# Kernel optimization log

Hardware: AMD Instinct MI355X
Metric: run time of the kernel (lower is better)

## Reference

```python
import jax, jax.numpy as jnp
import numpy as np
from jax import lax

B, CIN, HID, T, H, W = 4, 32, 32, 31, 96, 96


def setup_inputs() -> dict:
    key = jax.random.key(0)
    k1, k2, k3 = jax.random.split(key, 3)
    inputs = jax.random.normal(k1, (B, CIN, T, H, W), dtype=jnp.float32)
    conv_w = jax.random.normal(k2, (2 * HID, CIN, 3, 3, 3), dtype=jnp.float32) * 0.05
    conv_b = jax.random.normal(k3, (2 * HID,), dtype=jnp.float32) * 0.05
    gamma = jnp.ones((1,), dtype=jnp.float32)
    return {"inputs": inputs, "conv_w": conv_w, "conv_b": conv_b, "gamma": gamma}


def reference(inputs, conv_w, conv_b, gamma):
    hid = conv_w.shape[0] // 2
    # Conv3d, 'same' padding, NCDHW layout -> gates [B, 2*hid, T, H, W]
    gates = lax.conv_general_dilated(
        inputs, conv_w, window_strides=(1, 1, 1), padding="SAME",
        dimension_numbers=("NCDHW", "OIDHW", "NCDHW"))
    gates = gates + conv_b[None, :, None, None, None]
    Z = jnp.tanh(gates[:, :hid])          # [B, hid, T, H, W]
    F = jax.nn.sigmoid(gates[:, hid:])    # [B, hid, T, H, W]

    # Gated recurrence over time (dim 2): h_t = f_t * h_{t-1} + (1 - f_t) * z_t
    Zt = jnp.moveaxis(Z, 2, 0)  # [T, B, hid, H, W]
    Ft = jnp.moveaxis(F, 2, 0)

    def step(h, zf):
        z, f = zf
        h = f * h + (1.0 - f) * z
        return h, h

    h0 = jnp.zeros_like(Zt[0])  # h=None <=> h0=0 since f*0+(1-f)*z
    _, hs = lax.scan(step, h0, (Zt, Ft))
    h_time = jnp.moveaxis(hs, 0, 2)  # [B, hid, T, H, W]

    # Per-spatial-location channel attention
    qh = jnp.transpose(h_time, (0, 3, 4, 1, 2))  # [B, H, W, C, T]
    scores = jnp.einsum("bhwct,bhwdt->bhwcd", qh, qh)  # [B, H, W, C, C]
    attn = jax.nn.softmax(scores, axis=3)  # softmax over row axis c (dim=3), as in torch
    attn = attn * (1.0 / np.sqrt(qh.shape[-2]))  # divide AFTER softmax by sqrt(C)
    ah = jnp.einsum("bhwcd,bhwdt->bhwct", attn, qh)  # [B, H, W, C, T]
    ah = jnp.transpose(ah, (0, 3, 4, 1, 2))  # [B, C, T, H, W]

    return gamma * ah + h_time
```

## Files before the change

### kernel.cpp

```cpp
#include <hip/hip_runtime.h>
#include <math.h>

#define B_ 4
#define CIN_ 32
#define HID_ 32
#define T_ 31
#define H_ 96
#define W_ 96
#define SP_ (H_*W_)
#define TSP (T_ * SP_)

typedef _Float16 half8 __attribute__((ext_vector_type(8)));
typedef float f32x4 __attribute__((ext_vector_type(4)));
typedef float f32x16 __attribute__((ext_vector_type(16)));

static __device__ inline unsigned int packhh(float a, float b) {
  unsigned short ua = __builtin_bit_cast(unsigned short, (_Float16)a);
  unsigned short ub = __builtin_bit_cast(unsigned short, (_Float16)b);
  return (unsigned int)ua | ((unsigned int)ub << 16);
}

__global__ __launch_bounds__(256) void prep_w_kernel(
    const float* __restrict__ w, _Float16* __restrict__ wr) {
  int idx = blockIdx.x * 256 + threadIdx.x;
  if (idx >= 55296) return;
  int i = idx & 7;
  int lane = (idx >> 3) & 63;
  int rest = idx >> 9;
  int tap = rest % 27;
  int ocg = rest / 27;
  int m = lane & 15;
  int cin = (lane >> 4) * 8 + i;
  int oc = (m & 1) * 32 + ocg * 8 + (m >> 1);
  wr[idx] = (_Float16)(w[(oc * CIN_ + cin) * 27 + tap]);
}

#define PITCH 40
#define SROWS 8
#define SCOLS 18
#define RST (SCOLS * PITCH)
#define SLICE_HF (SROWS * RST)

__global__ __launch_bounds__(256, 2) void conv_rec_mfma(
    const float* __restrict__ in, const _Float16* __restrict__ wr,
    const float* __restrict__ bias, unsigned int* __restrict__ gout) {
  __shared__ _Float16 in_s[4 * SLICE_HF];

  const int tid = threadIdx.x;
  const int tile = blockIdx.x;
  const int b = blockIdx.y;
  const int x0 = (tile % 6) * 16;
  const int y0 = (tile / 6) * 6;
  const int lane = tid & 63;
  const int ocg = tid >> 6;
  const int px = lane & 15;
  const int kq = lane >> 4;

  half8 wreg[27];
  {
    const _Float16* wp = wr + (size_t)ocg * 27 * 512 + lane * 8;
#pragma unroll
    for (int tap = 0; tap < 27; ++tap)
      wreg[tap] = *(const half8*)(wp + tap * 512);
  }

  const int c0 = ocg * 8 + 2 * kq;
  f32x4 bias4;
  bias4[0] = bias[c0];
  bias4[1] = bias[32 + c0];
  bias4[2] = bias[c0 + 1];
  bias4[3] = bias[32 + c0 + 1];

  const int s_xi = tid & 15;
  const int s_q  = tid >> 4;
  const int ibase = s_q * TSP + (y0 - 1) * W_ + x0 + s_xi;
  const int wbase = (s_xi + 1) * PITCH + s_q;
  const int e_cin = tid & 31;
  const int e_yy  = tid >> 5;
  const int e_gy  = y0 - 1 + e_yy;
  const bool e_ok = ((unsigned)e_gy < (unsigned)H_);
  const int eoff  = e_cin * TSP + e_gy * W_;
  const int ew0   = e_yy * RST + 0 * PITCH + e_cin;
  const int ew1   = e_yy * RST + 17 * PITCH + e_cin;
  const bool has_l = (x0 > 0), has_r = (x0 + 16 < W_);

  int cs[3];
#pragma unroll
  for (int kw = 0; kw < 3; ++kw) cs[kw] = (px + kw) * PITCH + kq * 8;

  const float* inb = in + (size_t)(b * CIN_) * TSP;

  auto stage_full = [&](int ts) {
    _Float16* dst = in_s + (ts & 3) * SLICE_HF;
    const int tso = ts * SP_;
#pragma unroll
    for (int k = 0; k < 16; ++k) {
      const int gy = y0 - 1 + (k >> 1);
      float v = 0.f;
      if ((unsigned)gy < (unsigned)H_)
        v = inb[ibase + (k & 1) * 16 * TSP + (k >> 1) * W_ + tso];
      dst[wbase + (k >> 1) * RST + (k & 1) * 16] = (_Float16)v;
    }
    float v0 = 0.f, v1 = 0.f;
    if (e_ok) {
      if (has_l) v0 = inb[eoff + tso + x0 - 1];
      if (has_r) v1 = inb[eoff + tso + x0 + 16];
    }
    dst[ew0] = (_Float16)v0;
    dst[ew1] = (_Float16)v1;
  };

  {
    uint32_t* dz = (uint32_t*)(in_s + 3 * SLICE_HF);
    for (int e = tid; e < SLICE_HF / 2; e += 256) dz[e] = 0u;
  }
  stage_full(0);
  stage_full(1);
  __syncthreads();

  float h[6][2];
#pragma unroll
  for (int r = 0; r < 6; ++r) { h[r][0] = 0.f; h[r][1] = 0.f; }

  const int pr = ocg * 4 + kq;
  size_t obase = ((size_t)(b * 32 + pr) * T_) * SP_ + y0 * W_ + x0 + px;

  for (int t = 0; t < T_; ++t) {
    const int ts = t + 2;

    float sv[16], ev0 = 0.f, ev1 = 0.f;
    if (ts < T_) {
      const int tso = ts * SP_;
#pragma unroll
      for (int k = 0; k < 16; ++k) {
        const int gy = y0 - 1 + (k >> 1);
        sv[k] = 0.f;
        if ((unsigned)gy < (unsigned)H_)
          sv[k] = inb[ibase + (k & 1) * 16 * TSP + (k >> 1) * W_ + tso];
      }
      if (e_ok) {
        if (has_l) ev0 = inb[eoff + tso + x0 - 1];
        if (has_r) ev1 = inb[eoff + tso + x0 + 16];
      }
    }

    f32x4 acc[6];
#pragma unroll
    for (int r = 0; r < 6; ++r) acc[r] = bias4;

#pragma unroll
    for (int kd = 0; kd < 3; ++kd) {
      const _Float16* sb2 = in_s + ((t + 3 + kd) & 3) * SLICE_HF;
#pragma unroll
      for (int kw = 0; kw < 3; ++kw) {
        half8 brow[8];
#pragma unroll
        for (int rr = 0; rr < 8; ++rr)
          brow[rr] = *(const half8*)(sb2 + rr * RST + cs[kw]);
#pragma unroll
        for (int kh = 0; kh < 3; ++kh) {
          const int tap = kd * 9 + kh * 3 + kw;
#pragma unroll
          for (int r = 0; r < 6; ++r)
            acc[r] = __builtin_amdgcn_mfma_f32_16x16x32_f16(
                wreg[tap], brow[r + kh], acc[r], 0, 0, 0);
        }
      }
    }

    if (ts < T_) {
      _Float16* dst = in_s + (ts & 3) * SLICE_HF;
#pragma unroll
      for (int k = 0; k < 16; ++k)
        dst[wbase + (k >> 1) * RST + (k & 1) * 16] = (_Float16)sv[k];
      dst[ew0] = (_Float16)ev0;
      dst[ew1] = (_Float16)ev1;
    } else if (ts == T_) {
      uint32_t* dz = (uint32_t*)(in_s + (ts & 3) * SLICE_HF);
      for (int e = tid; e < SLICE_HF / 2; e += 256) dz[e] = 0u;
    }

    unsigned int pk[6];
#pragma unroll
    for (int r = 0; r < 6; ++r) {
      float z0 = 1.f - 2.f / (1.f + __expf(2.f * acc[r][0]));
      float f0 = 1.f / (1.f + __expf(-acc[r][1]));
      h[r][0] = f0 * (h[r][0] - z0) + z0;
      float z1 = 1.f - 2.f / (1.f + __expf(2.f * acc[r][2]));
      float f1 = 1.f / (1.f + __expf(-acc[r][3]));
      h[r][1] = f1 * (h[r][1] - z1) + z1;
      pk[r] = packhh(h[r][0], h[r][1]);
    }
    __syncthreads();

#pragma unroll
    for (int r = 0; r < 6; ++r)
      gout[obase + r * W_] = pk[r];
    obase += SP_;
  }
}

#define APIT 40
#define PSTR 1288

__global__ __launch_bounds__(512) void attn_mfma(
    unsigned int* __restrict__ g, const float* __restrict__ gamma) {
  __shared__ _Float16 qh_s[16 * PSTR];
  __shared__ _Float16 qt_s[16 * PSTR];
  __shared__ _Float16 at_s[8 * 32 * APIT];

  const int tid = threadIdx.x;
  const int x0 = blockIdx.x * 16;
  const int y = blockIdx.y;
  const int b = blockIdx.z;
  const int lane = tid & 63;
  const int wv = tid >> 6;
  const float gm = gamma[0];

  for (int e = tid; e < 16 * 16 * 31; e += 512) {
    int xi = e & 15;
    int q = e >> 4;
    int t = q % 31;
    int pr = q / 31;
    unsigned int gw = g[((size_t)(b * 32 + pr) * T_ + t) * SP_ + y * W_ + x0 + xi];
    _Float16 h0 = __builtin_bit_cast(_Float16, (unsigned short)(gw & 0xffff));
    _Float16 h1 = __builtin_bit_cast(_Float16, (unsigned short)(gw >> 16));
    int c0 = 2 * pr;
    qh_s[xi * PSTR + c0 * APIT + t] = h0;
    qh_s[xi * PSTR + (c0 + 1) * APIT + t] = h1;
    qt_s[xi * PSTR + t * APIT + c0] = h0;
    qt_s[xi * PSTR + t * APIT + c0 + 1] = h1;
  }
  qh_s[(tid & 15) * PSTR + (tid >> 4) * APIT + 31] = (_Float16)0.f;
  __syncthreads();

  const int cd = lane & 31;
  const int hi = lane >> 5;

#pragma unroll
  for (int pp = 0; pp < 2; ++pp) {
    const int px = wv * 2 + pp;
    const _Float16* qs = qh_s + px * PSTR;
    const _Float16* qt = qt_s + px * PSTR;
    _Float16* as = at_s + wv * (32 * APIT);

    half8 q0 = *(const half8*)(qs + cd * APIT + hi * 8);
    half8 q1 = *(const half8*)(qs + cd * APIT + hi * 8 + 16);
    f32x16 S = {};
    S = __builtin_amdgcn_mfma_f32_32x32x16_f16(q0, q0, S, 0, 0, 0);
    S = __builtin_amdgcn_mfma_f32_32x32x16_f16(q1, q1, S, 0, 0, 0);

    float mx = S[0];
#pragma unroll
    for (int r = 1; r < 16; ++r) mx = fmaxf(mx, S[r]);
    mx = fmaxf(mx, __shfl_xor(mx, 32));
    float sm = 0.f;
    float ev[16];
#pragma unroll
    for (int r = 0; r < 16; ++r) { ev[r] = __expf(S[r] - mx); sm += ev[r]; }
    sm += __shfl_xor(sm, 32);
    const float sc = 0.17677669529663688f / sm;

#pragma unroll
    for (int r = 0; r < 16; ++r) {
      int c = (r & 3) + 8 * (r >> 2) + 4 * hi;
      as[c * APIT + cd] = (_Float16)(ev[r] * sc);
    }

    half8 a0 = *(const half8*)(as + cd * APIT + hi * 8);
    half8 a1 = *(const half8*)(as + cd * APIT + hi * 8 + 16);
    half8 b0 = *(const half8*)(qt + cd * APIT + hi * 8);
    half8 b1 = *(const half8*)(qt + cd * APIT + hi * 8 + 16);
    f32x16 P = {};
    P = __builtin_amdgcn_mfma_f32_32x32x16_f16(a0, b0, P, 0, 0, 0);
    P = __builtin_amdgcn_mfma_f32_32x32x16_f16(a1, b1, P, 0, 0, 0);

#pragma unroll
    for (int r = 0; r < 16; ++r) {
      int c = (r & 3) + 8 * (r >> 2) + 4 * hi;
      qt_s[px * PSTR + cd * APIT + c] = (_Float16)P[r];
    }
  }
  __syncthreads();

  float* gf = (float*)g;
  for (int e = tid; e < 4 * 992; e += 512) {
    int xi4 = e & 3;
    int q = e >> 2;
    int t = q % 31;
    int c = q / 31;
    float4 rv;
#pragma unroll
    for (int j = 0; j < 4; ++j) {
      int xi = xi4 * 4 + j;
      float ah = (float)qt_s[xi * PSTR + t * APIT + c];
      float hv = (float)qh_s[xi * PSTR + c * APIT + t];
      (&rv.x)[j] = gm * ah + hv;
    }
    *(float4*)&gf[((size_t)(b * HID_ + c) * T_ + t) * SP_ + y * W_ + x0 +
                  xi4 * 4] = rv;
  }
}

extern "C" void kernel_launch(void* const* d_in, const int* in_sizes, int n_in,
                              void* d_out, int out_size, void* d_ws,
                              size_t ws_size, hipStream_t stream) {
  const float* in    = (const float*)d_in[0];
  const float* w     = (const float*)d_in[1];
  const float* bias  = (const float*)d_in[2];
  const float* gamma = (const float*)d_in[3];
  _Float16* wr = (_Float16*)d_ws;

  prep_w_kernel<<<216, 256, 0, stream>>>(w, wr);
  conv_rec_mfma<<<dim3(96, 4), 256, 0, stream>>>(
      in, wr, bias, (unsigned int*)d_out);
  attn_mfma<<<dim3(6, 96, 4), 512, 0, stream>>>(
      (unsigned int*)d_out, gamma);
}
```

Measured before the change: 270.3 us.

## Make attention kernel persistent with register prefetch of next tile

Changes the attention kernel from one block per 16-pixel tile to 256 persistent blocks. Each block loops over 9 tiles and loads the next tile's packed fp16 data into registers while the current tile is being computed. The large shared-memory footprint allows only about one block per CU, so this is meant to hide global load latency that previously could not be covered by other resident blocks. It also writes the transposed copy as one 32-bit store instead of two halves. The cost is higher register pressure and a fixed grid sized to the CU count, which can leave the work unevenly spread.

```diff
diff --git a/kernel.cpp b/kernel.cpp
--- a/kernel.cpp
+++ b/kernel.cpp
@@ -202,6 +202,8 @@
 
 #define APIT 40
 #define PSTR 1288
+#define NTILES 2304
+#define TPB 9
 
 __global__ __launch_bounds__(512) void attn_mfma(
     unsigned int* __restrict__ g, const float* __restrict__ gamma) {
@@ -210,95 +212,136 @@
   __shared__ _Float16 at_s[8 * 32 * APIT];
 
   const int tid = threadIdx.x;
-  const int x0 = blockIdx.x * 16;
-  const int y = blockIdx.y;
-  const int b = blockIdx.z;
+  const int bid = blockIdx.x;
   const int lane = tid & 63;
   const int wv = tid >> 6;
   const float gm = gamma[0];
-
-  for (int e = tid; e < 16 * 16 * 31; e += 512) {
-    int xi = e & 15;
-    int q = e >> 4;
-    int t = q % 31;
-    int pr = q / 31;
-    unsigned int gw = g[((size_t)(b * 32 + pr) * T_ + t) * SP_ + y * W_ + x0 + xi];
-    _Float16 h0 = __builtin_bit_cast(_Float16, (unsigned short)(gw & 0xffff));
-    _Float16 h1 = __builtin_bit_cast(_Float16, (unsigned short)(gw >> 16));
-    int c0 = 2 * pr;
-    qh_s[xi * PSTR + c0 * APIT + t] = h0;
-    qh_s[xi * PSTR + (c0 + 1) * APIT + t] = h1;
-    qt_s[xi * PSTR + t * APIT + c0] = h0;
-    qt_s[xi * PSTR + t * APIT + c0 + 1] = h1;
-  }
-  qh_s[(tid & 15) * PSTR + (tid >> 4) * APIT + 31] = (_Float16)0.f;
-  __syncthreads();
-
+  const int xi = tid & 15;
+  const int q0 = tid >> 4;
   const int cd = lane & 31;
   const int hi = lane >> 5;
 
-#pragma unroll
-  for (int pp = 0; pp < 2; ++pp) {
-    const int px = wv * 2 + pp;
-    const _Float16* qs = qh_s + px * PSTR;
-    const _Float16* qt = qt_s + px * PSTR;
-    _Float16* as = at_s + wv * (32 * APIT);
-
-    half8 q0 = *(const half8*)(qs + cd * APIT + hi * 8);
-    half8 q1 = *(const half8*)(qs + cd * APIT + hi * 8 + 16);
-    f32x16 S = {};
-    S = __builtin_amdgcn_mfma_f32_32x32x16_f16(q0, q0, S, 0, 0, 0);
-    S = __builtin_amdgcn_mfma_f32_32x32x16_f16(q1, q1, S, 0, 0, 0);
-
-    float mx = S[0];
-#pragma unroll
-    for (int r = 1; r < 16; ++r) mx = fmaxf(mx, S[r]);
-    mx = fmaxf(mx, __shfl_xor(mx, 32));
-    float sm = 0.f;
-    float ev[16];
-#pragma unroll
-    for (int r = 0; r < 16; ++r) { ev[r] = __expf(S[r] - mx); sm += ev[r]; }
-    sm += __shfl_xor(sm, 32);
-    const float sc = 0.17677669529663688f / sm;
-
-#pragma unroll
-    for (int r = 0; r < 16; ++r) {
-      int c = (r & 3) + 8 * (r >> 2) + 4 * hi;
-      as[c * APIT + cd] = (_Float16)(ev[r] * sc);
-    }
-
-    half8 a0 = *(const half8*)(as + cd * APIT + hi * 8);
-    half8 a1 = *(const half8*)(as + cd * APIT + hi * 8 + 16);
-    half8 b0 = *(const half8*)(qt + cd * APIT + hi * 8);
-    half8 b1 = *(const half8*)(qt + cd * APIT + hi * 8 + 16);
-    f32x16 P = {};
-    P = __builtin_amdgcn_mfma_f32_32x32x16_f16(a0, b0, P, 0, 0, 0);
-    P = __builtin_amdgcn_mfma_f32_32x32x16_f16(a1, b1, P, 0, 0, 0);
-
-#pragma unroll
-    for (int r = 0; r < 16; ++r) {
-      int c = (r & 3) + 8 * (r >> 2) + 4 * hi;
-      qt_s[px * PSTR + cd * APIT + c] = (_Float16)P[r];
-    }
-  }
-  __syncthreads();
-
-  float* gf = (float*)g;
-  for (int e = tid; e < 4 * 992; e += 512) {
-    int xi4 = e & 3;
-    int q = e >> 2;
-    int t = q % 31;
-    int c = q / 31;
-    float4 rv;
-#pragma unroll
-    for (int j = 0; j < 4; ++j) {
-      int xi = xi4 * 4 + j;
-      float ah = (float)qt_s[xi * PSTR + t * APIT + c];
-      float hv = (float)qh_s[xi * PSTR + c * APIT + t];
-      (&rv.x)[j] = gm * ah + hv;
-    }
-    *(float4*)&gf[((size_t)(b * HID_ + c) * T_ + t) * SP_ + y * W_ + x0 +
-                  xi4 * 4] = rv;
+  unsigned int sv[16];
+
+  {
+    int ti = bid;
+    int xt = ti % 6; int rem = ti / 6; int y = rem % 96; int b = rem / 96;
+    const unsigned int* gb =
+        g + (size_t)(b * 32) * TSP + y * W_ + xt * 16 + xi;
+#pragma unroll
+    for (int k2 = 0; k2 < 16; ++k2) {
+      int q = q0 + 32 * k2;
+      int t = q % 31;
+      int pr = q / 31;
+      if (q < 496) sv[k2] = gb[(size_t)(pr * T_ + t) * SP_];
+    }
+  }
+
+  int ti = bid;
+  for (int k = 0; k < TPB; ++k) {
+    const int xt = ti % 6;
+    const int rem = ti / 6;
+    const int y = rem % 96;
+    const int b = rem / 96;
+    const int x0 = xt * 16;
+
+#pragma unroll
+    for (int k2 = 0; k2 < 16; ++k2) {
+      int q = q0 + 32 * k2;
+      int t = q % 31;
+      int pr = q / 31;
+      if (q < 496) {
+        unsigned int gw = sv[k2];
+        _Float16 h0 = __builtin_bit_cast(_Float16, (unsigned short)(gw & 0xffff));
+        _Float16 h1 = __builtin_bit_cast(_Float16, (unsigned short)(gw >> 16));
+        int c0 = 2 * pr;
+        qh_s[xi * PSTR + c0 * APIT + t] = h0;
+        qh_s[xi * PSTR + (c0 + 1) * APIT + t] = h1;
+        *(unsigned int*)&qt_s[xi * PSTR + t * APIT + c0] = gw;
+      }
+    }
+    qh_s[xi * PSTR + q0 * APIT + 31] = (_Float16)0.f;
+
+    if (k + 1 < TPB) {
+      int tn = ti + 256;
+      int xt2 = tn % 6; int rem2 = tn / 6; int y2 = rem2 % 96; int b2 = rem2 / 96;
+      const unsigned int* gb =
+          g + (size_t)(b2 * 32) * TSP + y2 * W_ + xt2 * 16 + xi;
+#pragma unroll
+      for (int k2 = 0; k2 < 16; ++k2) {
+        int q = q0 + 32 * k2;
+        int t = q % 31;
+        int pr = q / 31;
+        if (q < 496) sv[k2] = gb[(size_t)(pr * T_ + t) * SP_];
+      }
+    }
+    __syncthreads();
+
+#pragma unroll
+    for (int pp = 0; pp < 2; ++pp) {
+      const int px = wv * 2 + pp;
+      const _Float16* qs = qh_s + px * PSTR;
+      const _Float16* qt = qt_s + px * PSTR;
+      _Float16* as = at_s + wv * (32 * APIT);
+
+      half8 a0q = *(const half8*)(qs + cd * APIT + hi * 8);
+      half8 a1q = *(const half8*)(qs + cd * APIT + hi * 8 + 16);
+      f32x16 S = {};
+      S = __builtin_amdgcn_mfma_f32_32x32x16_f16(a0q, a0q, S, 0, 0, 0);
+      S = __builtin_amdgcn_mfma_f32_32x32x16_f16(a1q, a1q, S, 0, 0, 0);
+
+      float mx = S[0];
+#pragma unroll
+      for (int r = 1; r < 16; ++r) mx = fmaxf(mx, S[r]);
+      mx = fmaxf(mx, __shfl_xor(mx, 32));
+      float sm = 0.f;
+      float ev[16];
+#pragma unroll
+      for (int r = 0; r < 16; ++r) { ev[r] = __expf(S[r] - mx); sm += ev[r]; }
+      sm += __shfl_xor(sm, 32);
+      const float sc = 0.17677669529663688f / sm;
+
+#pragma unroll
+      for (int r = 0; r < 16; ++r) {
+        int c = (r & 3) + 8 * (r >> 2) + 4 * hi;
+        as[c * APIT + cd] = (_Float16)(ev[r] * sc);
+      }
+
+      half8 a0 = *(const half8*)(as + cd * APIT + hi * 8);
+      half8 a1 = *(const half8*)(as + cd * APIT + hi * 8 + 16);
+      half8 b0 = *(const half8*)(qt + cd * APIT + hi * 8);
+      half8 b1 = *(const half8*)(qt + cd * APIT + hi * 8 + 16);
+      f32x16 P = {};
+      P = __builtin_amdgcn_mfma_f32_32x32x16_f16(a0, b0, P, 0, 0, 0);
+      P = __builtin_amdgcn_mfma_f32_32x32x16_f16(a1, b1, P, 0, 0, 0);
+
+#pragma unroll
+      for (int r = 0; r < 16; ++r) {
+        int c = (r & 3) + 8 * (r >> 2) + 4 * hi;
+        qt_s[px * PSTR + cd * APIT + c] = (_Float16)P[r];
+      }
+    }
+    __syncthreads();
+
+    float* gf = (float*)g;
+    for (int e = tid; e < 4 * 992; e += 512) {
+      int xi4 = e & 3;
+      int q = e >> 2;
+      int t = q % 31;
+      int c = q / 31;
+      float4 rv;
+#pragma unroll
+      for (int j = 0; j < 4; ++j) {
+        int x2 = xi4 * 4 + j;
+        float ah = (float)qt_s[x2 * PSTR + t * APIT + c];
+        float hv = (float)qh_s[x2 * PSTR + c * APIT + t];
+        (&rv.x)[j] = gm * ah + hv;
+      }
+      *(float4*)&gf[((size_t)(b * HID_ + c) * T_ + t) * SP_ + y * W_ + x0 +
+                    xi4 * 4] = rv;
+    }
+    ti += 256;
+    __syncthreads();
   }
 }
 
@@ -314,6 +357,6 @@
   prep_w_kernel<<<216, 256, 0, stream>>>(w, wr);
   conv_rec_mfma<<<dim3(96, 4), 256, 0, stream>>>(
       in, wr, bias, (unsigned int*)d_out);
-  attn_mfma<<<dim3(6, 96, 4), 512, 0, stream>>>(
+  attn_mfma<<<dim3(256), 512, 0, stream>>>(
       (unsigned int*)d_out, gamma);
 }
```

After: 231.7 us. 14.3% less time.
